# Kernel tuning notes

Hardware: AMD Instinct MI355X
Metric: run time of the kernel (lower is better)

Reference implementation:

```python
import jax, jax.numpy as jnp
import numpy as np

B, S, D, H, F = 4, 2048, 1024, 16, 4096
DH = D // H
EPS = 1e-6


def setup_inputs() -> dict:
    key = jax.random.key(0)
    ks = jax.random.split(key, 8)
    sc = 1.0 / np.sqrt(D)
    return {
        "x": jax.random.normal(ks[0], (B, S, D), jnp.float32),
        "wq": jax.random.normal(ks[1], (D, D), jnp.float32) * sc,
        "bq": jnp.zeros((D,), jnp.float32),
        "wk": jax.random.normal(ks[2], (D, D), jnp.float32) * sc,
        "bk": jnp.zeros((D,), jnp.float32),
        "wv": jax.random.normal(ks[3], (D, D), jnp.float32) * sc,
        "bv": jnp.zeros((D,), jnp.float32),
        "wo": jax.random.normal(ks[4], (D, D), jnp.float32) * sc,
        "bo": jnp.zeros((D,), jnp.float32),
        "w1": jax.random.normal(ks[5], (D, F), jnp.float32) * sc,
        "b1": jnp.zeros((F,), jnp.float32),
        "w2": jax.random.normal(ks[6], (F, D), jnp.float32) * (1.0 / np.sqrt(F)),
        "b2": jnp.zeros((D,), jnp.float32),
        "g1": jnp.ones((D,), jnp.float32),
        "be1": jnp.zeros((D,), jnp.float32),
        "g2": jnp.ones((D,), jnp.float32),
        "be2": jnp.zeros((D,), jnp.float32),
    }


def _layernorm(x, g, b):
    mu = jnp.mean(x, axis=-1, keepdims=True)
    var = jnp.mean(jnp.square(x - mu), axis=-1, keepdims=True)
    return (x - mu) * jax.lax.rsqrt(var + EPS) * g + b


def reference(x, wq, bq, wk, bk, wv, bv, wo, bo, w1, b1, w2, b2, g1, be1, g2, be2):
    # self-attention: q=k=v=x
    q = (x @ wq + bq).reshape(B, S, H, DH).transpose(0, 2, 1, 3)  # [B,H,S,DH]
    k = (x @ wk + bk).reshape(B, S, H, DH).transpose(0, 2, 1, 3)
    v = (x @ wv + bv).reshape(B, S, H, DH).transpose(0, 2, 1, 3)
    logits = jnp.einsum("bhqd,bhkd->bhqk", q, k) / jnp.sqrt(jnp.float32(DH))
    attn = jax.nn.softmax(logits, axis=-1)
    ctx = jnp.einsum("bhqk,bhkd->bhqd", attn, v)  # [B,H,S,DH]
    ctx = ctx.transpose(0, 2, 1, 3).reshape(B, S, D)
    attn_out = ctx @ wo + bo
    out1 = _layernorm(x + attn_out, g1, be1)
    ffn = jax.nn.relu(out1 @ w1 + b1) @ w2 + b2
    out2 = _layernorm(out1 + ffn, g2, be2)
    return out2
```

## Files before the change

### kernel.cpp

```cpp
#include <hip/hip_runtime.h>

typedef unsigned short u16;
typedef unsigned int u32;

typedef __attribute__((ext_vector_type(8))) short short8;
typedef __attribute__((ext_vector_type(4))) float floatx4;
typedef __attribute__((ext_vector_type(16))) float floatx16;
typedef __attribute__((ext_vector_type(2))) unsigned int uint2v;
typedef __attribute__((ext_vector_type(4))) unsigned int uint4v;

static __device__ __forceinline__ u16 f2b(float f) {
    union { float f; u32 i; } v; v.f = f;
    u32 r = v.i + 0x7fffu + ((v.i >> 16) & 1u);
    return (u16)(r >> 16);
}
static __device__ __forceinline__ float exp2f_hw(float x) {
    return __builtin_amdgcn_exp2f(x);
}
static __device__ __forceinline__ u32 cvtpk(float lo, float hi) {
    u32 r;
    asm("v_cvt_pk_bf16_f32 %0, %1, %2" : "=v"(r) : "v"(lo), "v"(hi));
    return r;
}

static __device__ __forceinline__ floatx4 mfma16(short8 a, short8 b, floatx4 c) {
    return __builtin_amdgcn_mfma_f32_16x16x32_bf16(a, b, c, 0, 0, 0);
}
static __device__ __forceinline__ floatx16 mfma32(short8 a, short8 b, floatx16 c) {
    return __builtin_amdgcn_mfma_f32_32x32x16_bf16(a, b, c, 0, 0, 0);
}

typedef __attribute__((address_space(1))) const void gas_void;
typedef __attribute__((address_space(3))) void las_void;
static __device__ __forceinline__ void gl_lds16(const void* g, void* l) {
    __builtin_amdgcn_global_load_lds((gas_void*)g, (las_void*)l, 16, 0, 0);
}

template<int N> static __device__ __forceinline__ void vmw() {
    if constexpr (N == 0)      asm volatile("s_waitcnt vmcnt(0)" ::: "memory");
    else if constexpr (N == 2) asm volatile("s_waitcnt vmcnt(2)" ::: "memory");
    else if constexpr (N == 4) asm volatile("s_waitcnt vmcnt(4)" ::: "memory");
}
#define SBAR() asm volatile("s_barrier" ::: "memory")

#define B_ 4
#define S_ 2048
#define D_ 1024
#define H_ 16
#define DH_ 64
#define F_ 4096
#define QKVS 3072

#define QSCALE 0.18033688011112042f

__global__ __launch_bounds__(256) void prep(
    const float* __restrict__ x, u16* __restrict__ xb,
    const float* __restrict__ wq, const float* __restrict__ wk,
    const float* __restrict__ wv, const float* __restrict__ wo,
    u16* __restrict__ wqkvT, u16* __restrict__ woT,
    const float* __restrict__ w1, u16* __restrict__ w1T,
    const float* __restrict__ w2, u16* __restrict__ w2T,
    const float* __restrict__ bq, const float* __restrict__ bk,
    const float* __restrict__ bv, float* __restrict__ qkvb) {
    int bid = blockIdx.x, tid = threadIdx.x;

    if (bid < 8192) {
        int id = bid * 256 + tid;
        float4 v = ((const float4*)x)[id];
        ushort4 u;
        u.x = f2b(v.x); u.y = f2b(v.y); u.z = f2b(v.z); u.w = f2b(v.w);
        ((ushort4*)xb)[id] = u;
        return;
    }
    bid -= 8192;

    if (bid >= 12288) {
        int i = (bid - 12288) * 256 + tid;
        float v;
        if (i < 1024) v = bq[i] * QSCALE;
        else if (i < 2048) v = bk[i - 1024];
        else v = bv[i - 2048];
        qkvb[i] = v;
        return;
    }

    __shared__ float t[32][33];
    int x32 = tid & 31, y8 = tid >> 5;
    const float* in; u16* outp; float scale = 1.0f; int R, C, bx, by;
    if (bid < 4096) {
        int z = bid >> 10, rem = bid & 1023;
        bx = rem & 31; by = rem >> 5;
        in = (z == 0) ? wq : (z == 1) ? wk : (z == 2) ? wv : wo;
        outp = (z == 0) ? wqkvT : (z == 1) ? (wqkvT + 1024 * 1024)
             : (z == 2) ? (wqkvT + 2048 * 1024) : woT;
        scale = (z == 0) ? QSCALE : 1.0f;
        R = 1024; C = 1024;
    } else if (bid < 8192) {
        int rem = bid - 4096; bx = rem & 127; by = rem >> 7;
        in = w1; outp = w1T; R = 1024; C = 4096;
    } else {
        int rem = bid - 8192; bx = rem & 31; by = rem >> 5;
        in = w2; outp = w2T; R = 4096; C = 1024;
    }
#pragma unroll
    for (int i = 0; i < 4; ++i) {
        int r = by * 32 + y8 + i * 8;
        t[y8 + i * 8][x32] = in[(size_t)r * C + bx * 32 + x32];
    }
    __syncthreads();
#pragma unroll
    for (int i = 0; i < 4; ++i) {
        int c = bx * 32 + y8 + i * 8;
        outp[(size_t)c * R + by * 32 + x32] = f2b(t[x32][y8 + i * 8] * scale);
    }
}

__global__ void transpose_v(const u16* __restrict__ qkv, u16* __restrict__ vt) {
    __shared__ u16 t[32][33];
    int bh = blockIdx.z; int b = bh >> 4, h = bh & 15;
    int s0 = blockIdx.x * 32, d0 = blockIdx.y * 32;
    int x = threadIdx.x, y = threadIdx.y;
#pragma unroll
    for (int i = 0; i < 4; ++i)
        t[y + i * 8][x] =
            qkv[(size_t)(b * S_ + s0 + y + i * 8) * QKVS + 2048 + h * DH_ + d0 + x];
    __syncthreads();
#pragma unroll
    for (int i = 0; i < 4; ++i)
        vt[((size_t)bh * DH_ + d0 + y + i * 8) * S_ + s0 + x] = t[x][y + i * 8];
}

#define MFMA16X(MH)                                                        \
    __builtin_amdgcn_s_setprio(1);                                         \
    acc[(MH)*4+0][0] = mfma16(af0, bf0, acc[(MH)*4+0][0]);                 \
    acc[(MH)*4+0][1] = mfma16(af0, bf1, acc[(MH)*4+0][1]);                 \
    acc[(MH)*4+0][2] = mfma16(af0, bf2, acc[(MH)*4+0][2]);                 \
    acc[(MH)*4+0][3] = mfma16(af0, bf3, acc[(MH)*4+0][3]);                 \
    acc[(MH)*4+1][0] = mfma16(af1, bf0, acc[(MH)*4+1][0]);                 \
    acc[(MH)*4+1][1] = mfma16(af1, bf1, acc[(MH)*4+1][1]);                 \
    acc[(MH)*4+1][2] = mfma16(af1, bf2, acc[(MH)*4+1][2]);                 \
    acc[(MH)*4+1][3] = mfma16(af1, bf3, acc[(MH)*4+1][3]);                 \
    acc[(MH)*4+2][0] = mfma16(af2, bf0, acc[(MH)*4+2][0]);                 \
    acc[(MH)*4+2][1] = mfma16(af2, bf1, acc[(MH)*4+2][1]);                 \
    acc[(MH)*4+2][2] = mfma16(af2, bf2, acc[(MH)*4+2][2]);                 \
    acc[(MH)*4+2][3] = mfma16(af2, bf3, acc[(MH)*4+2][3]);                 \
    acc[(MH)*4+3][0] = mfma16(af3, bf0, acc[(MH)*4+3][0]);                 \
    acc[(MH)*4+3][1] = mfma16(af3, bf1, acc[(MH)*4+3][1]);                 \
    acc[(MH)*4+3][2] = mfma16(af3, bf2, acc[(MH)*4+3][2]);                 \
    acc[(MH)*4+3][3] = mfma16(af3, bf3, acc[(MH)*4+3][3]);                 \
    __builtin_amdgcn_s_setprio(0);

#define PPAIR(P, KH, STa, Wa, STb, Wb) {                                   \
    int ro = l * 64 + ((((KH) * 4 + quad) ^ l7) << 3);                     \
    const u16* bBp = &smem[32768 + (P) * 16384 + wc * 4096];               \
    short8 bf0 = *(const short8*)&bBp[ro];                                 \
    short8 bf1 = *(const short8*)&bBp[ro + 1024];                          \
    short8 bf2 = *(const short8*)&bBp[ro + 2048];                          \
    short8 bf3 = *(const short8*)&bBp[ro + 3072];                          \
    {   const u16* bAp = &smem[(P) * 16384 + (wr * 2 + 0) * 4096];         \
        short8 af0 = *(const short8*)&bAp[ro];                             \
        short8 af1 = *(const short8*)&bAp[ro + 1024];                      \
        short8 af2 = *(const short8*)&bAp[ro + 2048];                      \
        short8 af3 = *(const short8*)&bAp[ro + 3072];                      \
        STa; Wa;                                                           \
        MFMA16X(0)                                                         \
        SBAR();                                                            \
    }                                                                      \
    {   const u16* bAp = &smem[(P) * 16384 + (wr * 2 + 1) * 4096];         \
        short8 af0 = *(const short8*)&bAp[ro];                             \
        short8 af1 = *(const short8*)&bAp[ro + 1024];                      \
        short8 af2 = *(const short8*)&bAp[ro + 2048];                      \
        short8 af3 = *(const short8*)&bAp[ro + 3072];                      \
        STb; Wb;                                                           \
        MFMA16X(1)                                                         \
        SBAR();                                                            \
    } }

__global__ __launch_bounds__(512) void gemm256(const u16* __restrict__ A,
                                               const u16* __restrict__ Bt,
                                               const float* __restrict__ bias,
                                               float* __restrict__ outF,
                                               float* __restrict__ outF2,
                                               u16* __restrict__ outB,
                                               int M, int N, int K, int klen,
                                               int relu) {
    __shared__ __align__(16) u16 smem[65536];

    int tid = threadIdx.x;
    int w = tid >> 6, lane = tid & 63, quad = lane >> 4, l = lane & 15;
    int wr = w >> 2, wc = w & 3;
    int l7 = l & 7;

    int nbN = gridDim.x, nwg = gridDim.x * gridDim.y;
    int flat = blockIdx.y * gridDim.x + blockIdx.x;
    int swz = (flat & 7) * (nwg >> 3) + (flat >> 3);
    int bM = swz / nbN, bN = swz % nbN;
    int koff = blockIdx.z * klen;

    floatx4 acc[8][4];
#pragma unroll
    for (int i = 0; i < 8; ++i)
#pragma unroll
        for (int j = 0; j < 4; ++j) acc[i][j] = (floatx4){0.f, 0.f, 0.f, 0.f};

    int rT = tid >> 3, cT = tid & 7;
    int cg8 = ((cT ^ (rT & 7)) << 3);
    const u16* gA0 = A + (size_t)(bM * 256 + rT) * K + koff + cg8;
    const u16* gB0 = Bt + (size_t)(bN * 256 + rT) * K + koff + cg8;

    auto stA = [&](int p, int ch, int t) {
        gl_lds16(gA0 + (size_t)(ch * 64) * K + t * 64,
                 (void*)&smem[p * 16384 + ch * 4096 + (w << 9)]);
    };
    auto stB = [&](int p, int hb, int t) {
        gl_lds16(gB0 + (size_t)(hb * 64) * K + t * 64,
                 (void*)&smem[32768 + p * 16384 + hb * 4096 + (w << 9)]);
    };

    stA(0, 0, 0); stA(0, 1, 0); stA(0, 2, 0); stA(0, 3, 0);
    stB(0, 0, 0); stB(0, 1, 0); stB(0, 2, 0); stB(0, 3, 0);
    stA(1, 0, 1); stA(1, 2, 1);
    vmw<2>(); SBAR();

    const int NI = klen >> 7;
    for (int j = 0; j < NI - 1; ++j) {
        int to = 2 * j + 1, te = 2 * j + 2, tn = 2 * j + 3;
        PPAIR(0, 0, (stA(1,1,to), stA(1,3,to), stB(1,0,to), stB(1,1,to)), ((void)0),
                    (stB(1,2,to), stB(1,3,to)), ((void)0))
        PPAIR(0, 1, ((void)0), ((void)0),
                    (stA(0,0,te), stA(0,2,te)), vmw<2>())
        PPAIR(1, 0, (stA(0,1,te), stA(0,3,te), stB(0,0,te), stB(0,1,te)), ((void)0),
                    (stB(0,2,te), stB(0,3,te)), ((void)0))
        PPAIR(1, 1, ((void)0), ((void)0),
                    (stA(1,0,tn), stA(1,2,tn)), vmw<2>())
    }
    {
        int to = 2 * (NI - 1) + 1;
        PPAIR(0, 0, (stA(1,1,to), stA(1,3,to), stB(1,0,to), stB(1,1,to)), ((void)0),
                    (stB(1,2,to), stB(1,3,to)), ((void)0))
        PPAIR(0, 1, ((void)0), ((void)0), ((void)0), vmw<0>())
        PPAIR(1, 0, ((void)0), ((void)0), ((void)0), ((void)0))
        PPAIR(1, 1, ((void)0), ((void)0), ((void)0), ((void)0))
    }

    float* of = (blockIdx.z == 0) ? outF : outF2;
    const float* bp = (blockIdx.z == 0) ? bias : nullptr;
    float bv4[4];
#pragma unroll
    for (int nt = 0; nt < 4; ++nt) {
        int colg = bN * 256 + wc * 64 + nt * 16 + l;
        bv4[nt] = bp ? bp[colg] : 0.f;
    }
#pragma unroll
    for (int mt = 0; mt < 8; ++mt) {
#pragma unroll
        for (int rr = 0; rr < 4; ++rr) {
            int rowg = bM * 256 + wr * 128 + mt * 16 + quad * 4 + rr;
            size_t rb = (size_t)rowg * N + bN * 256 + wc * 64 + l;
#pragma unroll
            for (int nt = 0; nt < 4; ++nt) {
                float v = acc[mt][nt][rr] + bv4[nt];
                if (relu) v = fmaxf(v, 0.f);
                if (of) of[rb + nt * 16] = v;
                if (outB) outB[rb + nt * 16] = f2b(v);
            }
        }
    }
}

#define PACK8(sv, rb, dst) {                                                   \
    u32 pa_ = cvtpk(sv[rb + 0], sv[rb + 1]), pb_ = cvtpk(sv[rb + 4], sv[rb + 5]); \
    u32 pc_ = cvtpk(sv[rb + 2], sv[rb + 3]), pd_ = cvtpk(sv[rb + 6], sv[rb + 7]); \
    uint2v t0_ = __builtin_amdgcn_permlane32_swap(pa_, pb_, 0, 0);             \
    uint2v t1_ = __builtin_amdgcn_permlane32_swap(pc_, pd_, 0, 0);             \
    union { uint4v u; short8 s8; } cv_;                                        \
    cv_.u = (uint4v){t0_[0], t1_[0], t0_[1], t1_[1]};                          \
    dst = cv_.s8; }

__global__ __launch_bounds__(256, 2) void attn_kernel(const u16* __restrict__ qkv,
                                                      const u16* __restrict__ vt,
                                                      u16* __restrict__ ctx) {
    __shared__ __align__(16) u16 Kb[2][64 * 64];
    __shared__ __align__(16) u16 Vb[2][64 * 64];

    int bh = blockIdx.x; int b = bh >> 4, h = bh & 15;
    int tid = threadIdx.x;
    int w = tid >> 6, lane = tid & 63;
    int l32 = lane & 31, hi = lane >> 5, row7 = lane & 7;
    int qw = blockIdx.y * 256 + w * 64;

    int r = lane >> 3, c = lane & 7;
    int cs = ((c ^ r) << 3);
    const u16* gK0 = qkv + (size_t)(b * S_ + w * 16 + r) * QKVS + 1024 + h * DH_ + cs;
    const u16* gK1 = gK0 + (size_t)8 * QKVS;
    const u16* gV0 = vt + (size_t)(bh * DH_ + w * 16 + r) * S_ + cs;
    const u16* gV1 = gV0 + (size_t)8 * S_;

    auto stage = [&](int bb) {
        u16* lk = &Kb[bb][w * 16 * 64];
        u16* lv = &Vb[bb][w * 16 * 64];
        gl_lds16(gK0, lk);
        gl_lds16(gK1, lk + 8 * 64);
        gl_lds16(gV0, lv);
        gl_lds16(gV1, lv + 8 * 64);
        gK0 += (size_t)64 * QKVS; gK1 += (size_t)64 * QKVS;
        gV0 += 64; gV1 += 64;
    };

    short8 qa0, qa1, qa2, qa3, qb0, qb1, qb2, qb3;
    {
        const u16* qpA = qkv + (size_t)(b * S_ + qw + l32) * QKVS + h * DH_ + hi * 8;
        qa0 = *(const short8*)(qpA);
        qa1 = *(const short8*)(qpA + 16);
        qa2 = *(const short8*)(qpA + 32);
        qa3 = *(const short8*)(qpA + 48);
        const u16* qpB = qpA + (size_t)32 * QKVS;
        qb0 = *(const short8*)(qpB);
        qb1 = *(const short8*)(qpB + 16);
        qb2 = *(const short8*)(qpB + 32);
        qb3 = *(const short8*)(qpB + 48);
    }

    floatx16 OA0, OA1, OB0, OB1;
#pragma unroll
    for (int i = 0; i < 16; ++i) { OA0[i] = 0.f; OA1[i] = 0.f; OB0[i] = 0.f; OB1[i] = 0.f; }
    float lra0 = 0.f, lra1 = 0.f, lrb0 = 0.f, lrb1 = 0.f;

    int roff0 = l32 * 64;
    int roff1 = (32 + l32) * 64;

    stage(0);
    __syncthreads();

    const int NT = S_ / 64;
    for (int kt = 0; kt < NT; ++kt) {
        int cur = kt & 1;
        if (kt + 1 < NT) stage(cur ^ 1);

        const u16* Kc = Kb[cur];
        const u16* Vc = Vb[cur];

        short8 paA0, paA1, paA2, paA3, paB0, paB1, paB2, paB3;

        {
            floatx16 sA, sB;
#pragma unroll
            for (int i = 0; i < 16; ++i) { sA[i] = 0.f; sB[i] = 0.f; }
#pragma unroll
            for (int kc = 0; kc < 4; ++kc) {
                int ch = (((kc * 2 + hi) ^ row7) << 3);
                short8 ka = *(const short8*)&Kc[roff0 + ch];
                short8 qkA = (kc == 0) ? qa0 : (kc == 1) ? qa1 : (kc == 2) ? qa2 : qa3;
                short8 qkB = (kc == 0) ? qb0 : (kc == 1) ? qb1 : (kc == 2) ? qb2 : qb3;
                sA = mfma32(ka, qkA, sA);
                sB = mfma32(ka, qkB, sB);
            }
#pragma unroll
            for (int i = 0; i < 16; ++i) { sA[i] = exp2f_hw(sA[i]); sB[i] = exp2f_hw(sB[i]); }
#pragma unroll
            for (int i = 0; i < 16; i += 4) {
                lra0 += sA[i + 0] + sA[i + 1];
                lra1 += sA[i + 2] + sA[i + 3];
                lrb0 += sB[i + 0] + sB[i + 1];
                lrb1 += sB[i + 2] + sB[i + 3];
            }
            PACK8(sA, 0, paA0); PACK8(sA, 8, paA1);
            PACK8(sB, 0, paB0); PACK8(sB, 8, paB1);
        }

        {
            floatx16 sA, sB;
#pragma unroll
            for (int i = 0; i < 16; ++i) { sA[i] = 0.f; sB[i] = 0.f; }
#pragma unroll
            for (int kc = 0; kc < 4; ++kc) {
                int ch = (((kc * 2 + hi) ^ row7) << 3);
                short8 ka = *(const short8*)&Kc[roff1 + ch];
                short8 qkA = (kc == 0) ? qa0 : (kc == 1) ? qa1 : (kc == 2) ? qa2 : qa3;
                short8 qkB = (kc == 0) ? qb0 : (kc == 1) ? qb1 : (kc == 2) ? qb2 : qb3;
                sA = mfma32(ka, qkA, sA);
                sB = mfma32(ka, qkB, sB);
            }
#pragma unroll
            for (int i = 0; i < 16; ++i) { sA[i] = exp2f_hw(sA[i]); sB[i] = exp2f_hw(sB[i]); }
#pragma unroll
            for (int i = 0; i < 16; i += 4) {
                lra0 += sA[i + 0] + sA[i + 1];
                lra1 += sA[i + 2] + sA[i + 3];
                lrb0 += sB[i + 0] + sB[i + 1];
                lrb1 += sB[i + 2] + sB[i + 3];
            }
            PACK8(sA, 0, paA2); PACK8(sA, 8, paA3);
            PACK8(sB, 0, paB2); PACK8(sB, 8, paB3);
        }

        {
            short8 vb0 = *(const short8*)&Vc[roff0 + (((0 + hi) ^ row7) << 3)];
            OA0 = mfma32(paA0, vb0, OA0);
            OB0 = mfma32(paB0, vb0, OB0);
            short8 vb1 = *(const short8*)&Vc[roff0 + (((2 + hi) ^ row7) << 3)];
            OA0 = mfma32(paA1, vb1, OA0);
            OB0 = mfma32(paB1, vb1, OB0);
            short8 vb2 = *(const short8*)&Vc[roff0 + (((4 + hi) ^ row7) << 3)];
            OA0 = mfma32(paA2, vb2, OA0);
            OB0 = mfma32(paB2, vb2, OB0);
            short8 vb3 = *(const short8*)&Vc[roff0 + (((6 + hi) ^ row7) << 3)];
            OA0 = mfma32(paA3, vb3, OA0);
            OB0 = mfma32(paB3, vb3, OB0);
        }
        {
            short8 vb0 = *(const short8*)&Vc[roff1 + (((0 + hi) ^ row7) << 3)];
            OA1 = mfma32(paA0, vb0, OA1);
            OB1 = mfma32(paB0, vb0, OB1);
            short8 vb1 = *(const short8*)&Vc[roff1 + (((2 + hi) ^ row7) << 3)];
            OA1 = mfma32(paA1, vb1, OA1);
            OB1 = mfma32(paB1, vb1, OB1);
            short8 vb2 = *(const short8*)&Vc[roff1 + (((4 + hi) ^ row7) << 3)];
            OA1 = mfma32(paA2, vb2, OA1);
            OB1 = mfma32(paB2, vb2, OB1);
            short8 vb3 = *(const short8*)&Vc[roff1 + (((6 + hi) ^ row7) << 3)];
            OA1 = mfma32(paA3, vb3, OA1);
            OB1 = mfma32(paB3, vb3, OB1);
        }

        __syncthreads();
    }

    float lrA = lra0 + lra1;
    float lrB = lrb0 + lrb1;
    lrA += __shfl_xor(lrA, 32);
    lrB += __shfl_xor(lrB, 32);
    float invA = 1.0f / lrA;
    float invB = 1.0f / lrB;
#pragma unroll
    for (int rr = 0; rr < 16; ++rr) {
        int rowq = (rr & 3) + 8 * (rr >> 2) + 4 * hi;
        float ivA = __shfl(invA, rowq);
        float ivB = __shfl(invB, rowq);
        size_t baseA = (size_t)(b * S_ + qw + rowq) * D_ + h * DH_ + l32;
        ctx[baseA]      = f2b(OA0[rr] * ivA);
        ctx[baseA + 32] = f2b(OA1[rr] * ivA);
        size_t baseB = baseA + (size_t)32 * D_;
        ctx[baseB]      = f2b(OB0[rr] * ivB);
        ctx[baseB + 32] = f2b(OB1[rr] * ivB);
    }
}

__global__ __launch_bounds__(256) void add_ln3(const float* __restrict__ a,
                                               const float* __restrict__ b,
                                               const float* __restrict__ c,
                                               const float* __restrict__ g,
                                               const float* __restrict__ be,
                                               float* __restrict__ outF,
                                               u16* __restrict__ outB) {
    int row = blockIdx.x, tid = threadIdx.x;
    size_t base = (size_t)row * D_;
    float4 va = ((const float4*)(a + base))[tid];
    float4 vb = ((const float4*)(b + base))[tid];
    float4 vc = ((const float4*)(c + base))[tid];
    float x0 = va.x + vb.x + vc.x, x1 = va.y + vb.y + vc.y;
    float x2 = va.z + vb.z + vc.z, x3 = va.w + vb.w + vc.w;
    float s1 = x0 + x1 + x2 + x3;
    float s2 = x0 * x0 + x1 * x1 + x2 * x2 + x3 * x3;
#pragma unroll
    for (int off = 32; off; off >>= 1) {
        s1 += __shfl_xor(s1, off);
        s2 += __shfl_xor(s2, off);
    }
    __shared__ float r1[4], r2[4];
    int w = tid >> 6, lane = tid & 63;
    if (lane == 0) { r1[w] = s1; r2[w] = s2; }
    __syncthreads();
    s1 = r1[0] + r1[1] + r1[2] + r1[3];
    s2 = r2[0] + r2[1] + r2[2] + r2[3];
    float mean = s1 * (1.0f / D_);
    float var = s2 * (1.0f / D_) - mean * mean;
    float inv = rsqrtf(var + 1e-6f);
    float4 vg = ((const float4*)g)[tid];
    float4 vbe = ((const float4*)be)[tid];
    float o0 = (x0 - mean) * inv * vg.x + vbe.x;
    float o1 = (x1 - mean) * inv * vg.y + vbe.y;
    float o2 = (x2 - mean) * inv * vg.z + vbe.z;
    float o3 = (x3 - mean) * inv * vg.w + vbe.w;
    float4 o; o.x = o0; o.y = o1; o.z = o2; o.w = o3;
    ((float4*)(outF + base))[tid] = o;
    if (outB) {
        ushort4 u;
        u.x = f2b(o0); u.y = f2b(o1); u.z = f2b(o2); u.w = f2b(o3);
        ((ushort4*)(outB + base))[tid] = u;
    }
}

extern "C" void kernel_launch(void* const* d_in, const int* in_sizes, int n_in,
                              void* d_out, int out_size, void* d_ws, size_t ws_size,
                              hipStream_t stream) {
    const float* x   = (const float*)d_in[0];
    const float* wq  = (const float*)d_in[1];
    const float* bq  = (const float*)d_in[2];
    const float* wk  = (const float*)d_in[3];
    const float* bk  = (const float*)d_in[4];
    const float* wv  = (const float*)d_in[5];
    const float* bv  = (const float*)d_in[6];
    const float* wo  = (const float*)d_in[7];
    const float* bo  = (const float*)d_in[8];
    const float* w1  = (const float*)d_in[9];
    const float* b1  = (const float*)d_in[10];
    const float* w2  = (const float*)d_in[11];
    const float* b2  = (const float*)d_in[12];
    const float* g1  = (const float*)d_in[13];
    const float* be1 = (const float*)d_in[14];
    const float* g2  = (const float*)d_in[15];
    const float* be2 = (const float*)d_in[16];
    float* out = (float*)d_out;
    char* ws = (char*)d_ws;
    const size_t MB = 1u << 20;

    u16* xb      = (u16*)(ws + 0);
    u16* wqkvT   = (u16*)(ws + 16 * MB);
    u16* woT     = (u16*)(ws + 22 * MB);
    u16* w1T     = (u16*)(ws + 24 * MB);
    u16* w2T     = (u16*)(ws + 32 * MB);
    float* qkvb  = (float*)(ws + 40 * MB);
    u16* qkv     = (u16*)(ws + 41 * MB);
    u16* vtb     = (u16*)(ws + 89 * MB);
    u16* ctxb    = (u16*)(ws + 105 * MB);
    float* attn_out = (float*)(ws + 121 * MB);
    float* out1     = (float*)(ws + 153 * MB);
    u16* out1b   = (u16*)(ws + 0);
    float* woP1  = (float*)(ws + 41 * MB);
    u16* hidden  = (u16*)(ws + 41 * MB);
    float* ffn2p0 = (float*)(ws + 121 * MB);

    prep<<<20492, 256, 0, stream>>>(x, xb, wq, wk, wv, wo, wqkvT, woT,
                                    w1, w1T, w2, w2T, bq, bk, bv, qkvb);

    gemm256<<<dim3(12, 32, 1), 512, 0, stream>>>(xb, wqkvT, qkvb, nullptr, nullptr,
                                                 qkv, B_ * S_, QKVS, D_, D_, 0);
    transpose_v<<<dim3(S_ / 32, DH_ / 32, B_ * H_), dim3(32, 8), 0, stream>>>(qkv, vtb);

    attn_kernel<<<dim3(B_ * H_, S_ / 256), 256, 0, stream>>>(qkv, vtb, ctxb);

    gemm256<<<dim3(4, 32, 2), 512, 0, stream>>>(ctxb, woT, bo, attn_out, woP1,
                                                nullptr, B_ * S_, D_, D_, D_ / 2, 0);
    add_ln3<<<B_ * S_, 256, 0, stream>>>(x, attn_out, woP1, g1, be1, out1, out1b);

    gemm256<<<dim3(16, 32, 1), 512, 0, stream>>>(out1b, w1T, b1, nullptr, nullptr,
                                                 hidden, B_ * S_, F_, D_, D_, 1);
    gemm256<<<dim3(4, 32, 2), 512, 0, stream>>>(hidden, w2T, b2, ffn2p0, out,
                                                nullptr, B_ * S_, D_, F_, F_ / 2, 0);
    add_ln3<<<B_ * S_, 256, 0, stream>>>(out1, ffn2p0, out, g2, be2, out, nullptr);
}
```

Before: 488.3 us.

## Replace split-K N=1024 GEMMs with 256x128-tile kernel, drop partial-sum reduction

Replaces the split-K (z=2) 256x256-tile GEMMs for the output projection and FFN down-projection with a new 256x128-tile kernel that walks the full K, giving 256 workgroups without splitting K. This removes the second fp32 partial-sum buffer write and the three-input add in layernorm, which now adds only two inputs. The trade-off is lower arithmetic intensity per tile (B tile halved) and a longer K loop per workgroup.

Result: faster. 478.5 us (-2.0%).

```diff
diff --git a/kernel.cpp b/kernel.cpp
--- a/kernel.cpp
+++ b/kernel.cpp
@@ -180,10 +180,8 @@
                                                const u16* __restrict__ Bt,
                                                const float* __restrict__ bias,
                                                float* __restrict__ outF,
-                                               float* __restrict__ outF2,
                                                u16* __restrict__ outB,
-                                               int M, int N, int K, int klen,
-                                               int relu) {
+                                               int M, int N, int K, int relu) {
     __shared__ __align__(16) u16 smem[65536];
 
     int tid = threadIdx.x;
@@ -195,7 +193,6 @@
     int flat = blockIdx.y * gridDim.x + blockIdx.x;
     int swz = (flat & 7) * (nwg >> 3) + (flat >> 3);
     int bM = swz / nbN, bN = swz % nbN;
-    int koff = blockIdx.z * klen;
 
     floatx4 acc[8][4];
 #pragma unroll
@@ -205,8 +202,8 @@
 
     int rT = tid >> 3, cT = tid & 7;
     int cg8 = ((cT ^ (rT & 7)) << 3);
-    const u16* gA0 = A + (size_t)(bM * 256 + rT) * K + koff + cg8;
-    const u16* gB0 = Bt + (size_t)(bN * 256 + rT) * K + koff + cg8;
+    const u16* gA0 = A + (size_t)(bM * 256 + rT) * K + cg8;
+    const u16* gB0 = Bt + (size_t)(bN * 256 + rT) * K + cg8;
 
     auto stA = [&](int p, int ch, int t) {
         gl_lds16(gA0 + (size_t)(ch * 64) * K + t * 64,
@@ -222,7 +219,7 @@
     stA(1, 0, 1); stA(1, 2, 1);
     vmw<2>(); SBAR();
 
-    const int NI = klen >> 7;
+    const int NI = K >> 7;
     for (int j = 0; j < NI - 1; ++j) {
         int to = 2 * j + 1, te = 2 * j + 2, tn = 2 * j + 3;
         PPAIR(0, 0, (stA(1,1,to), stA(1,3,to), stB(1,0,to), stB(1,1,to)), ((void)0),
@@ -243,13 +240,11 @@
         PPAIR(1, 1, ((void)0), ((void)0), ((void)0), ((void)0))
     }
 
-    float* of = (blockIdx.z == 0) ? outF : outF2;
-    const float* bp = (blockIdx.z == 0) ? bias : nullptr;
     float bv4[4];
 #pragma unroll
     for (int nt = 0; nt < 4; ++nt) {
         int colg = bN * 256 + wc * 64 + nt * 16 + l;
-        bv4[nt] = bp ? bp[colg] : 0.f;
+        bv4[nt] = bias ? bias[colg] : 0.f;
     }
 #pragma unroll
     for (int mt = 0; mt < 8; ++mt) {
@@ -261,7 +256,132 @@
             for (int nt = 0; nt < 4; ++nt) {
                 float v = acc[mt][nt][rr] + bv4[nt];
                 if (relu) v = fmaxf(v, 0.f);
-                if (of) of[rb + nt * 16] = v;
+                if (outF) outF[rb + nt * 16] = v;
+                if (outB) outB[rb + nt * 16] = f2b(v);
+            }
+        }
+    }
+}
+
+#define MFMA8X(MH)                                                         \
+    __builtin_amdgcn_s_setprio(1);                                         \
+    acc[(MH)*4+0][0] = mfma16(af0, bf0, acc[(MH)*4+0][0]);                 \
+    acc[(MH)*4+0][1] = mfma16(af0, bf1, acc[(MH)*4+0][1]);                 \
+    acc[(MH)*4+1][0] = mfma16(af1, bf0, acc[(MH)*4+1][0]);                 \
+    acc[(MH)*4+1][1] = mfma16(af1, bf1, acc[(MH)*4+1][1]);                 \
+    acc[(MH)*4+2][0] = mfma16(af2, bf0, acc[(MH)*4+2][0]);                 \
+    acc[(MH)*4+2][1] = mfma16(af2, bf1, acc[(MH)*4+2][1]);                 \
+    acc[(MH)*4+3][0] = mfma16(af3, bf0, acc[(MH)*4+3][0]);                 \
+    acc[(MH)*4+3][1] = mfma16(af3, bf1, acc[(MH)*4+3][1]);                 \
+    __builtin_amdgcn_s_setprio(0);
+
+#define PPAIRB(P, KH, STa, Wa, STb, Wb) {                                  \
+    int sw = (((KH) * 4 + quad) ^ l7) << 3;                                \
+    int ro = l * 64 + sw;                                                  \
+    int rob = ((wc & 1) * 32 + l) * 64 + sw;                               \
+    const u16* bBp = &smem[32768 + (P) * 8192 + (wc >> 1) * 4096];         \
+    short8 bf0 = *(const short8*)&bBp[rob];                                \
+    short8 bf1 = *(const short8*)&bBp[rob + 1024];                         \
+    {   const u16* bAp = &smem[(P) * 16384 + (wr * 2 + 0) * 4096];         \
+        short8 af0 = *(const short8*)&bAp[ro];                             \
+        short8 af1 = *(const short8*)&bAp[ro + 1024];                      \
+        short8 af2 = *(const short8*)&bAp[ro + 2048];                      \
+        short8 af3 = *(const short8*)&bAp[ro + 3072];                      \
+        STa; Wa;                                                           \
+        MFMA8X(0)                                                          \
+        SBAR();                                                            \
+    }                                                                      \
+    {   const u16* bAp = &smem[(P) * 16384 + (wr * 2 + 1) * 4096];         \
+        short8 af0 = *(const short8*)&bAp[ro];                             \
+        short8 af1 = *(const short8*)&bAp[ro + 1024];                      \
+        short8 af2 = *(const short8*)&bAp[ro + 2048];                      \
+        short8 af3 = *(const short8*)&bAp[ro + 3072];                      \
+        STb; Wb;                                                           \
+        MFMA8X(1)                                                          \
+        SBAR();                                                            \
+    } }
+
+__global__ __launch_bounds__(512) void gemm256b(const u16* __restrict__ A,
+                                                const u16* __restrict__ Bt,
+                                                const float* __restrict__ bias,
+                                                float* __restrict__ outF,
+                                                u16* __restrict__ outB,
+                                                int M, int N, int K, int relu) {
+    __shared__ __align__(16) u16 smem[49152];
+
+    int tid = threadIdx.x;
+    int w = tid >> 6, lane = tid & 63, quad = lane >> 4, l = lane & 15;
+    int wr = w >> 2, wc = w & 3;
+    int l7 = l & 7;
+
+    int nbN = gridDim.x, nwg = gridDim.x * gridDim.y;
+    int flat = blockIdx.y * gridDim.x + blockIdx.x;
+    int swz = (flat & 7) * (nwg >> 3) + (flat >> 3);
+    int bM = swz / nbN, bN = swz % nbN;
+
+    floatx4 acc[8][2];
+#pragma unroll
+    for (int i = 0; i < 8; ++i)
+#pragma unroll
+        for (int j = 0; j < 2; ++j) acc[i][j] = (floatx4){0.f, 0.f, 0.f, 0.f};
+
+    int rT = tid >> 3, cT = tid & 7;
+    int cg8 = ((cT ^ (rT & 7)) << 3);
+    const u16* gA0 = A + (size_t)(bM * 256 + rT) * K + cg8;
+    const u16* gB0 = Bt + (size_t)(bN * 128 + rT) * K + cg8;
+
+    auto stA = [&](int p, int ch, int t) {
+        gl_lds16(gA0 + (size_t)(ch * 64) * K + t * 64,
+                 (void*)&smem[p * 16384 + ch * 4096 + (w << 9)]);
+    };
+    auto stB = [&](int p, int hb, int t) {
+        gl_lds16(gB0 + (size_t)(hb * 64) * K + t * 64,
+                 (void*)&smem[32768 + p * 8192 + hb * 4096 + (w << 9)]);
+    };
+
+    stA(0, 0, 0); stA(0, 1, 0); stA(0, 2, 0); stA(0, 3, 0);
+    stB(0, 0, 0); stB(0, 1, 0);
+    stA(1, 0, 1); stA(1, 2, 1);
+    vmw<2>(); SBAR();
+
+    const int NI = K >> 7;
+    for (int j = 0; j < NI - 1; ++j) {
+        int to = 2 * j + 1, te = 2 * j + 2, tn = 2 * j + 3;
+        PPAIRB(0, 0, (stA(1,1,to), stA(1,3,to), stB(1,0,to), stB(1,1,to)), ((void)0),
+                     ((void)0), ((void)0))
+        PPAIRB(0, 1, ((void)0), ((void)0),
+                     (stA(0,0,te), stA(0,2,te)), vmw<2>())
+        PPAIRB(1, 0, (stA(0,1,te), stA(0,3,te), stB(0,0,te), stB(0,1,te)), ((void)0),
+                     ((void)0), ((void)0))
+        PPAIRB(1, 1, ((void)0), ((void)0),
+                     (stA(1,0,tn), stA(1,2,tn)), vmw<2>())
+    }
+    {
+        int to = 2 * (NI - 1) + 1;
+        PPAIRB(0, 0, (stA(1,1,to), stA(1,3,to), stB(1,0,to), stB(1,1,to)), ((void)0),
+                     ((void)0), ((void)0))
+        PPAIRB(0, 1, ((void)0), ((void)0), ((void)0), vmw<0>())
+        PPAIRB(1, 0, ((void)0), ((void)0), ((void)0), ((void)0))
+        PPAIRB(1, 1, ((void)0), ((void)0), ((void)0), ((void)0))
+    }
+
+    float bv2[2];
+#pragma unroll
+    for (int nt = 0; nt < 2; ++nt) {
+        int colg = bN * 128 + wc * 32 + nt * 16 + l;
+        bv2[nt] = bias ? bias[colg] : 0.f;
+    }
+#pragma unroll
+    for (int mt = 0; mt < 8; ++mt) {
+#pragma unroll
+        for (int rr = 0; rr < 4; ++rr) {
+            int rowg = bM * 256 + wr * 128 + mt * 16 + quad * 4 + rr;
+            size_t rb = (size_t)rowg * N + bN * 128 + wc * 32 + l;
+#pragma unroll
+            for (int nt = 0; nt < 2; ++nt) {
+                float v = acc[mt][nt][rr] + bv2[nt];
+                if (relu) v = fmaxf(v, 0.f);
+                if (outF) outF[rb + nt * 16] = v;
                 if (outB) outB[rb + nt * 16] = f2b(v);
             }
         }
@@ -446,20 +566,17 @@
     }
 }
 
-__global__ __launch_bounds__(256) void add_ln3(const float* __restrict__ a,
-                                               const float* __restrict__ b,
-                                               const float* __restrict__ c,
-                                               const float* __restrict__ g,
-                                               const float* __restrict__ be,
-                                               float* __restrict__ outF,
-                                               u16* __restrict__ outB) {
+__global__ __launch_bounds__(256) void add_ln(const float* __restrict__ a,
+                                              const float* __restrict__ b,
+                                              const float* __restrict__ g,
+                                              const float* __restrict__ be,
+                                              float* __restrict__ outF,
+                                              u16* __restrict__ outB) {
     int row = blockIdx.x, tid = threadIdx.x;
     size_t base = (size_t)row * D_;
     float4 va = ((const float4*)(a + base))[tid];
     float4 vb = ((const float4*)(b + base))[tid];
-    float4 vc = ((const float4*)(c + base))[tid];
-    float x0 = va.x + vb.x + vc.x, x1 = va.y + vb.y + vc.y;
-    float x2 = va.z + vb.z + vc.z, x3 = va.w + vb.w + vc.w;
+    float x0 = va.x + vb.x, x1 = va.y + vb.y, x2 = va.z + vb.z, x3 = va.w + vb.w;
     float s1 = x0 + x1 + x2 + x3;
     float s2 = x0 * x0 + x1 * x1 + x2 * x2 + x3 * x3;
 #pragma unroll
@@ -527,26 +644,25 @@
     float* attn_out = (float*)(ws + 121 * MB);
     float* out1     = (float*)(ws + 153 * MB);
     u16* out1b   = (u16*)(ws + 0);
-    float* woP1  = (float*)(ws + 41 * MB);
     u16* hidden  = (u16*)(ws + 41 * MB);
-    float* ffn2p0 = (float*)(ws + 121 * MB);
+    float* ffn2out = (float*)(ws + 121 * MB);
 
     prep<<<20492, 256, 0, stream>>>(x, xb, wq, wk, wv, wo, wqkvT, woT,
                                     w1, w1T, w2, w2T, bq, bk, bv, qkvb);
 
-    gemm256<<<dim3(12, 32, 1), 512, 0, stream>>>(xb, wqkvT, qkvb, nullptr, nullptr,
-                                                 qkv, B_ * S_, QKVS, D_, D_, 0);
+    gemm256<<<dim3(12, 32), 512, 0, stream>>>(xb, wqkvT, qkvb, nullptr, qkv,
+                                              B_ * S_, QKVS, D_, 0);
     transpose_v<<<dim3(S_ / 32, DH_ / 32, B_ * H_), dim3(32, 8), 0, stream>>>(qkv, vtb);
 
     attn_kernel<<<dim3(B_ * H_, S_ / 256), 256, 0, stream>>>(qkv, vtb, ctxb);
 
-    gemm256<<<dim3(4, 32, 2), 512, 0, stream>>>(ctxb, woT, bo, attn_out, woP1,
-                                                nullptr, B_ * S_, D_, D_, D_ / 2, 0);
-    add_ln3<<<B_ * S_, 256, 0, stream>>>(x, attn_out, woP1, g1, be1, out1, out1b);
-
-    gemm256<<<dim3(16, 32, 1), 512, 0, stream>>>(out1b, w1T, b1, nullptr, nullptr,
-                                                 hidden, B_ * S_, F_, D_, D_, 1);
-    gemm256<<<dim3(4, 32, 2), 512, 0, stream>>>(hidden, w2T, b2, ffn2p0, out,
-                                                nullptr, B_ * S_, D_, F_, F_ / 2, 0);
-    add_ln3<<<B_ * S_, 256, 0, stream>>>(out1, ffn2p0, out, g2, be2, out, nullptr);
-}
+    gemm256b<<<dim3(8, 32), 512, 0, stream>>>(ctxb, woT, bo, attn_out, nullptr,
+                                              B_ * S_, D_, D_, 0);
+    add_ln<<<B_ * S_, 256, 0, stream>>>(x, attn_out, g1, be1, out1, out1b);
+
+    gemm256<<<dim3(16, 32), 512, 0, stream>>>(out1b, w1T, b1, nullptr, hidden,
+                                              B_ * S_, F_, D_, 1);
+    gemm256b<<<dim3(8, 32), 512, 0, stream>>>(hidden, w2T, b2, ffn2out, nullptr,
+                                              B_ * S_, D_, F_, 0);
+    add_ln<<<B_ * S_, 256, 0, stream>>>(out1, ffn2out, g2, be2, out, nullptr);
+}
```

## Shrink GEMM tiles to 256x128 and drop split-K with three-way LayerNorm sum

Applied to the files above, without the earlier changes.

The GEMM tile narrows from 256x256 to 256x128, which halves the B-operand LDS buffers and the accumulators and doubles the number of workgroups. Split-K for the output projection and the second FFN GEMM is removed, since the smaller tiles already give enough blocks to fill the CUs. The LayerNorm kernels therefore sum two inputs instead of three, which drops one partial-result write and read. The cost is less data reuse per tile (more global and LDS traffic per FLOP) and lower MFMA density per wave between barriers.

Result: no change. 486.4 us (-0.4%).

```diff
diff --git a/kernel.cpp b/kernel.cpp
--- a/kernel.cpp
+++ b/kernel.cpp
@@ -130,40 +130,32 @@
         vt[((size_t)bh * DH_ + d0 + y + i * 8) * S_ + s0 + x] = t[x][y + i * 8];
 }
 
-#define MFMA16X(MH)                                                        \
+#define MFMA8X(MH)                                                         \
     __builtin_amdgcn_s_setprio(1);                                         \
     acc[(MH)*4+0][0] = mfma16(af0, bf0, acc[(MH)*4+0][0]);                 \
     acc[(MH)*4+0][1] = mfma16(af0, bf1, acc[(MH)*4+0][1]);                 \
-    acc[(MH)*4+0][2] = mfma16(af0, bf2, acc[(MH)*4+0][2]);                 \
-    acc[(MH)*4+0][3] = mfma16(af0, bf3, acc[(MH)*4+0][3]);                 \
     acc[(MH)*4+1][0] = mfma16(af1, bf0, acc[(MH)*4+1][0]);                 \
     acc[(MH)*4+1][1] = mfma16(af1, bf1, acc[(MH)*4+1][1]);                 \
-    acc[(MH)*4+1][2] = mfma16(af1, bf2, acc[(MH)*4+1][2]);                 \
-    acc[(MH)*4+1][3] = mfma16(af1, bf3, acc[(MH)*4+1][3]);                 \
     acc[(MH)*4+2][0] = mfma16(af2, bf0, acc[(MH)*4+2][0]);                 \
     acc[(MH)*4+2][1] = mfma16(af2, bf1, acc[(MH)*4+2][1]);                 \
-    acc[(MH)*4+2][2] = mfma16(af2, bf2, acc[(MH)*4+2][2]);                 \
-    acc[(MH)*4+2][3] = mfma16(af2, bf3, acc[(MH)*4+2][3]);                 \
     acc[(MH)*4+3][0] = mfma16(af3, bf0, acc[(MH)*4+3][0]);                 \
     acc[(MH)*4+3][1] = mfma16(af3, bf1, acc[(MH)*4+3][1]);                 \
-    acc[(MH)*4+3][2] = mfma16(af3, bf2, acc[(MH)*4+3][2]);                 \
-    acc[(MH)*4+3][3] = mfma16(af3, bf3, acc[(MH)*4+3][3]);                 \
     __builtin_amdgcn_s_setprio(0);
 
-#define PPAIR(P, KH, STa, Wa, STb, Wb) {                                   \
-    int ro = l * 64 + ((((KH) * 4 + quad) ^ l7) << 3);                     \
-    const u16* bBp = &smem[32768 + (P) * 16384 + wc * 4096];               \
-    short8 bf0 = *(const short8*)&bBp[ro];                                 \
-    short8 bf1 = *(const short8*)&bBp[ro + 1024];                          \
-    short8 bf2 = *(const short8*)&bBp[ro + 2048];                          \
-    short8 bf3 = *(const short8*)&bBp[ro + 3072];                          \
+#define PPAIRB(P, KH, STa, Wa, STb, Wb) {                                  \
+    int sw = (((KH) * 4 + quad) ^ l7) << 3;                                \
+    int ro = l * 64 + sw;                                                  \
+    int rob = ((wc & 1) * 32 + l) * 64 + sw;                               \
+    const u16* bBp = &smem[32768 + (P) * 8192 + (wc >> 1) * 4096];         \
+    short8 bf0 = *(const short8*)&bBp[rob];                                \
+    short8 bf1 = *(const short8*)&bBp[rob + 1024];                         \
     {   const u16* bAp = &smem[(P) * 16384 + (wr * 2 + 0) * 4096];         \
         short8 af0 = *(const short8*)&bAp[ro];                             \
         short8 af1 = *(const short8*)&bAp[ro + 1024];                      \
         short8 af2 = *(const short8*)&bAp[ro + 2048];                      \
         short8 af3 = *(const short8*)&bAp[ro + 3072];                      \
         STa; Wa;                                                           \
-        MFMA16X(0)                                                         \
+        MFMA8X(0)                                                          \
         SBAR();                                                            \
     }                                                                      \
     {   const u16* bAp = &smem[(P) * 16384 + (wr * 2 + 1) * 4096];         \
@@ -172,19 +164,17 @@
         short8 af2 = *(const short8*)&bAp[ro + 2048];                      \
         short8 af3 = *(const short8*)&bAp[ro + 3072];                      \
         STb; Wb;                                                           \
-        MFMA16X(1)                                                         \
+        MFMA8X(1)                                                          \
         SBAR();                                                            \
     } }
 
-__global__ __launch_bounds__(512) void gemm256(const u16* __restrict__ A,
-                                               const u16* __restrict__ Bt,
-                                               const float* __restrict__ bias,
-                                               float* __restrict__ outF,
-                                               float* __restrict__ outF2,
-                                               u16* __restrict__ outB,
-                                               int M, int N, int K, int klen,
-                                               int relu) {
-    __shared__ __align__(16) u16 smem[65536];
+__global__ __launch_bounds__(512) void gemm256b(const u16* __restrict__ A,
+                                                const u16* __restrict__ Bt,
+                                                const float* __restrict__ bias,
+                                                float* __restrict__ outF,
+                                                u16* __restrict__ outB,
+                                                int M, int N, int K, int relu) {
+    __shared__ __align__(16) u16 smem[49152];
 
     int tid = threadIdx.x;
     int w = tid >> 6, lane = tid & 63, quad = lane >> 4, l = lane & 15;
@@ -195,18 +185,17 @@
     int flat = blockIdx.y * gridDim.x + blockIdx.x;
     int swz = (flat & 7) * (nwg >> 3) + (flat >> 3);
     int bM = swz / nbN, bN = swz % nbN;
-    int koff = blockIdx.z * klen;
-
-    floatx4 acc[8][4];
+
+    floatx4 acc[8][2];
 #pragma unroll
     for (int i = 0; i < 8; ++i)
 #pragma unroll
-        for (int j = 0; j < 4; ++j) acc[i][j] = (floatx4){0.f, 0.f, 0.f, 0.f};
+        for (int j = 0; j < 2; ++j) acc[i][j] = (floatx4){0.f, 0.f, 0.f, 0.f};
 
     int rT = tid >> 3, cT = tid & 7;
     int cg8 = ((cT ^ (rT & 7)) << 3);
-    const u16* gA0 = A + (size_t)(bM * 256 + rT) * K + koff + cg8;
-    const u16* gB0 = Bt + (size_t)(bN * 256 + rT) * K + koff + cg8;
+    const u16* gA0 = A + (size_t)(bM * 256 + rT) * K + cg8;
+    const u16* gB0 = Bt + (size_t)(bN * 128 + rT) * K + cg8;
 
     auto stA = [&](int p, int ch, int t) {
         gl_lds16(gA0 + (size_t)(ch * 64) * K + t * 64,
@@ -214,54 +203,52 @@
     };
     auto stB = [&](int p, int hb, int t) {
         gl_lds16(gB0 + (size_t)(hb * 64) * K + t * 64,
-                 (void*)&smem[32768 + p * 16384 + hb * 4096 + (w << 9)]);
+                 (void*)&smem[32768 + p * 8192 + hb * 4096 + (w << 9)]);
     };
 
     stA(0, 0, 0); stA(0, 1, 0); stA(0, 2, 0); stA(0, 3, 0);
-    stB(0, 0, 0); stB(0, 1, 0); stB(0, 2, 0); stB(0, 3, 0);
+    stB(0, 0, 0); stB(0, 1, 0);
     stA(1, 0, 1); stA(1, 2, 1);
     vmw<2>(); SBAR();
 
-    const int NI = klen >> 7;
+    const int NI = K >> 7;
     for (int j = 0; j < NI - 1; ++j) {
         int to = 2 * j + 1, te = 2 * j + 2, tn = 2 * j + 3;
-        PPAIR(0, 0, (stA(1,1,to), stA(1,3,to), stB(1,0,to), stB(1,1,to)), ((void)0),
-                    (stB(1,2,to), stB(1,3,to)), ((void)0))
-        PPAIR(0, 1, ((void)0), ((void)0),
-                    (stA(0,0,te), stA(0,2,te)), vmw<2>())
-        PPAIR(1, 0, (stA(0,1,te), stA(0,3,te), stB(0,0,te), stB(0,1,te)), ((void)0),
-                    (stB(0,2,te), stB(0,3,te)), ((void)0))
-        PPAIR(1, 1, ((void)0), ((void)0),
-                    (stA(1,0,tn), stA(1,2,tn)), vmw<2>())
+        PPAIRB(0, 0, (stA(1,1,to), stA(1,3,to), stB(1,0,to), stB(1,1,to)), ((void)0),
+                     ((void)0), ((void)0))
+        PPAIRB(0, 1, ((void)0), ((void)0),
+                     (stA(0,0,te), stA(0,2,te)), vmw<2>())
+        PPAIRB(1, 0, (stA(0,1,te), stA(0,3,te), stB(0,0,te), stB(0,1,te)), ((void)0),
+                     ((void)0), ((void)0))
+        PPAIRB(1, 1, ((void)0), ((void)0),
+                     (stA(1,0,tn), stA(1,2,tn)), vmw<2>())
     }
     {
         int to = 2 * (NI - 1) + 1;
-        PPAIR(0, 0, (stA(1,1,to), stA(1,3,to), stB(1,0,to), stB(1,1,to)), ((void)0),
-                    (stB(1,2,to), stB(1,3,to)), ((void)0))
-        PPAIR(0, 1, ((void)0), ((void)0), ((void)0), vmw<0>())
-        PPAIR(1, 0, ((void)0), ((void)0), ((void)0), ((void)0))
-        PPAIR(1, 1, ((void)0), ((void)0), ((void)0), ((void)0))
-    }
-
-    float* of = (blockIdx.z == 0) ? outF : outF2;
-    const float* bp = (blockIdx.z == 0) ? bias : nullptr;
-    float bv4[4];
-#pragma unroll
-    for (int nt = 0; nt < 4; ++nt) {
-        int colg = bN * 256 + wc * 64 + nt * 16 + l;
-        bv4[nt] = bp ? bp[colg] : 0.f;
+        PPAIRB(0, 0, (stA(1,1,to), stA(1,3,to), stB(1,0,to), stB(1,1,to)), ((void)0),
+                     ((void)0), ((void)0))
+        PPAIRB(0, 1, ((void)0), ((void)0), ((void)0), vmw<0>())
+        PPAIRB(1, 0, ((void)0), ((void)0), ((void)0), ((void)0))
+        PPAIRB(1, 1, ((void)0), ((void)0), ((void)0), ((void)0))
+    }
+
+    float bv2[2];
+#pragma unroll
+    for (int nt = 0; nt < 2; ++nt) {
+        int colg = bN * 128 + wc * 32 + nt * 16 + l;
+        bv2[nt] = bias ? bias[colg] : 0.f;
     }
 #pragma unroll
     for (int mt = 0; mt < 8; ++mt) {
 #pragma unroll
         for (int rr = 0; rr < 4; ++rr) {
             int rowg = bM * 256 + wr * 128 + mt * 16 + quad * 4 + rr;
-            size_t rb = (size_t)rowg * N + bN * 256 + wc * 64 + l;
-#pragma unroll
-            for (int nt = 0; nt < 4; ++nt) {
-                float v = acc[mt][nt][rr] + bv4[nt];
+            size_t rb = (size_t)rowg * N + bN * 128 + wc * 32 + l;
+#pragma unroll
+            for (int nt = 0; nt < 2; ++nt) {
+                float v = acc[mt][nt][rr] + bv2[nt];
                 if (relu) v = fmaxf(v, 0.f);
-                if (of) of[rb + nt * 16] = v;
+                if (outF) outF[rb + nt * 16] = v;
                 if (outB) outB[rb + nt * 16] = f2b(v);
             }
         }
@@ -446,20 +433,17 @@
     }
 }
 
-__global__ __launch_bounds__(256) void add_ln3(const float* __restrict__ a,
-                                               const float* __restrict__ b,
-                                               const float* __restrict__ c,
-                                               const float* __restrict__ g,
-                                               const float* __restrict__ be,
-                                               float* __restrict__ outF,
-                                               u16* __restrict__ outB) {
+__global__ __launch_bounds__(256) void add_ln(const float* __restrict__ a,
+                                              const float* __restrict__ b,
+                                              const float* __restrict__ g,
+                                              const float* __restrict__ be,
+                                              float* __restrict__ outF,
+                                              u16* __restrict__ outB) {
     int row = blockIdx.x, tid = threadIdx.x;
     size_t base = (size_t)row * D_;
     float4 va = ((const float4*)(a + base))[tid];
     float4 vb = ((const float4*)(b + base))[tid];
-    float4 vc = ((const float4*)(c + base))[tid];
-    float x0 = va.x + vb.x + vc.x, x1 = va.y + vb.y + vc.y;
-    float x2 = va.z + vb.z + vc.z, x3 = va.w + vb.w + vc.w;
+    float x0 = va.x + vb.x, x1 = va.y + vb.y, x2 = va.z + vb.z, x3 = va.w + vb.w;
     float s1 = x0 + x1 + x2 + x3;
     float s2 = x0 * x0 + x1 * x1 + x2 * x2 + x3 * x3;
 #pragma unroll
@@ -527,26 +511,25 @@
     float* attn_out = (float*)(ws + 121 * MB);
     float* out1     = (float*)(ws + 153 * MB);
     u16* out1b   = (u16*)(ws + 0);
-    float* woP1  = (float*)(ws + 41 * MB);
     u16* hidden  = (u16*)(ws + 41 * MB);
-    float* ffn2p0 = (float*)(ws + 121 * MB);
+    float* ffn2out = (float*)(ws + 121 * MB);
 
     prep<<<20492, 256, 0, stream>>>(x, xb, wq, wk, wv, wo, wqkvT, woT,
                                     w1, w1T, w2, w2T, bq, bk, bv, qkvb);
 
-    gemm256<<<dim3(12, 32, 1), 512, 0, stream>>>(xb, wqkvT, qkvb, nullptr, nullptr,
-                                                 qkv, B_ * S_, QKVS, D_, D_, 0);
+    gemm256b<<<dim3(24, 32), 512, 0, stream>>>(xb, wqkvT, qkvb, nullptr, qkv,
+                                               B_ * S_, QKVS, D_, 0);
     transpose_v<<<dim3(S_ / 32, DH_ / 32, B_ * H_), dim3(32, 8), 0, stream>>>(qkv, vtb);
 
     attn_kernel<<<dim3(B_ * H_, S_ / 256), 256, 0, stream>>>(qkv, vtb, ctxb);
 
-    gemm256<<<dim3(4, 32, 2), 512, 0, stream>>>(ctxb, woT, bo, attn_out, woP1,
-                                                nullptr, B_ * S_, D_, D_, D_ / 2, 0);
-    add_ln3<<<B_ * S_, 256, 0, stream>>>(x, attn_out, woP1, g1, be1, out1, out1b);
-
-    gemm256<<<dim3(16, 32, 1), 512, 0, stream>>>(out1b, w1T, b1, nullptr, nullptr,
-                                                 hidden, B_ * S_, F_, D_, D_, 1);
-    gemm256<<<dim3(4, 32, 2), 512, 0, stream>>>(hidden, w2T, b2, ffn2p0, out,
-                                                nullptr, B_ * S_, D_, F_, F_ / 2, 0);
-    add_ln3<<<B_ * S_, 256, 0, stream>>>(out1, ffn2p0, out, g2, be2, out, nullptr);
-}
+    gemm256b<<<dim3(8, 32), 512, 0, stream>>>(ctxb, woT, bo, attn_out, nullptr,
+                                              B_ * S_, D_, D_, 0);
+    add_ln<<<B_ * S_, 256, 0, stream>>>(x, attn_out, g1, be1, out1, out1b);
+
+    gemm256b<<<dim3(32, 32), 512, 0, stream>>>(out1b, w1T, b1, nullptr, hidden,
+                                               B_ * S_, F_, D_, 1);
+    gemm256b<<<dim3(8, 32), 512, 0, stream>>>(hidden, w2T, b2, ffn2out, nullptr,
+                                              B_ * S_, D_, F_, 0);
+    add_ln<<<B_ * S_, 256, 0, stream>>>(out1, ffn2out, g2, be2, out, nullptr);
+}
```
